# Performance work log

Measured on AMD Instinct MI355X. Metric: run time of the kernel, lower is better.

## Reference

```python
import jax, jax.numpy as jnp
import numpy as np

N, D, NUM_CLASSES = 8192, 64, 16
EPS = 1e-7


def setup_inputs() -> dict:
    key = jax.random.key(0)
    k1, k2 = jax.random.split(key)
    raw = jax.random.normal(k1, (N, D), dtype=jnp.float32)
    # project into the open Poincare ball: norm < 0.9
    nrm = jnp.linalg.norm(raw, axis=-1, keepdims=True)
    points = raw * (0.9 / (1.0 + nrm))
    labels = jax.random.randint(k2, (N,), 0, NUM_CLASSES, dtype=jnp.int64)
    return {"points": points, "labels": labels}


def _poincare_dist_matrix(x):
    # d(x,y) = arccosh(1 + 2||x-y||^2 / ((1-||x||^2)(1-||y||^2)))
    sq = jnp.sum(x * x, axis=-1)                      # [N]
    sqdist = jnp.maximum(sq[:, None] + sq[None, :] - 2.0 * (x @ x.T), 0.0)  # [N,N]
    denom = jnp.maximum((1.0 - sq)[:, None] * (1.0 - sq)[None, :], EPS)
    arg = jnp.maximum(1.0 + 2.0 * sqdist / denom, 1.0 + EPS)
    return jnp.arccosh(arg)


def reference(points, labels):
    d = _poincare_dist_matrix(points)                 # [N,N]
    logits = -d
    n = logits.shape[0]
    diag = jnp.eye(n, dtype=bool)
    neg_inf = jnp.finfo(logits.dtype).min
    # log A_i = logsumexp_{a != i} (-d_ia)
    logA = jax.nn.logsumexp(jnp.where(diag, neg_inf, logits), axis=1)  # [N]
    pos = (labels[:, None] == labels[None, :]) & (~diag)               # [N,N]
    P = jnp.sum(pos, axis=1).astype(logits.dtype)                      # [N]
    p_sum = jnp.sum(jnp.where(pos, logits - logA[:, None], 0.0), axis=1)
    return jnp.sum(-p_sum / P)
```

## Files before the change

### kernel.cpp

```cpp
#include <hip/hip_runtime.h>

#define NPTS 8192
#define DIM 64
#define EPSF 1e-7f
#define LN2F 0.69314718055994531f
#define NBLK 1056

typedef unsigned short u16;
typedef __attribute__((ext_vector_type(8))) short bf16x8;
typedef __attribute__((ext_vector_type(8))) unsigned short u16x8;
typedef __attribute__((ext_vector_type(4))) float f32x4;

__global__ void prep_kernel(const float* __restrict__ x,
                            u16* __restrict__ hi, u16* __restrict__ lo,
                            float* __restrict__ hsq, float* __restrict__ rcpom,
                            float* __restrict__ m4r,
                            float* __restrict__ S, float* __restrict__ T,
                            float* __restrict__ out) {
    int g = blockIdx.x * blockDim.x + threadIdx.x;
    int row = g >> 3, sub = g & 7;
    const float* xp = x + row * DIM + sub * 8;
    float v[8];
    float s = 0.f;
#pragma unroll
    for (int k = 0; k < 8; k++) { v[k] = xp[k]; s = fmaf(v[k], v[k], s); }
    s += __shfl_xor(s, 1);
    s += __shfl_xor(s, 2);
    s += __shfl_xor(s, 4);
    u16x8 h, l;
#pragma unroll
    for (int k = 0; k < 8; k++) {
        unsigned int bits = __float_as_uint(v[k]);
        u16 hb = (u16)(bits >> 16);
        float hf = __uint_as_float(((unsigned int)hb) << 16);
        float lf = v[k] - hf;
        u16 lb = (u16)(__float_as_uint(lf) >> 16);
        h[k] = hb; l[k] = lb;
    }
    *(u16x8*)(hi + row * DIM + sub * 8) = h;
    *(u16x8*)(lo + row * DIM + sub * 8) = l;
    if (sub == 0) {
        float r = 1.0f / (1.0f - s);
        hsq[row] = -0.5f * s;
        rcpom[row] = r;
        m4r[row] = -4.0f * r;
    } else if (sub == 1) {
        S[row] = 0.f;
    } else if (sub == 2) {
        T[row] = 0.f;
    }
    if (g == 3) out[0] = 0.f;
}

__device__ __forceinline__ int cumtiles(int b) { return 65 * b - b * b; }

__global__ void __launch_bounds__(256, 3) pair_mfma(
        const u16* __restrict__ hi, const u16* __restrict__ lo,
        const float* __restrict__ hsq, const float* __restrict__ rcpom,
        const float* __restrict__ m4r, const int* __restrict__ labels,
        float* __restrict__ Sarr, float* __restrict__ Tarr) {
    __shared__ float slabS[4][256], slabT[4][256];

    int tid = threadIdx.x;
    int bid = blockIdx.x;
    int by = (int)((65.0f - __builtin_amdgcn_sqrtf(4225.0f - 4.0f * (float)bid)) * 0.5f);
    while (cumtiles(by + 1) <= bid) by++;
    while (cumtiles(by) > bid) by--;
    int off = bid - cumtiles(by);
    int bx = 2 * by + off;
    bool full = (off >= 2);

    int wave = tid >> 6, lane = tid & 63;
    int quad = lane >> 4, l15 = lane & 15;
    int i0 = bx * 128 + wave * 32;
    int j0 = by * 256;

    bf16x8 a_hi[2][2], a_lo[2][2];
#pragma unroll
    for (int it = 0; it < 2; it++)
#pragma unroll
        for (int ks = 0; ks < 2; ks++) {
            int aoff = (i0 + it * 16 + l15) * DIM + ks * 32 + quad * 8;
            a_hi[it][ks] = *(const bf16x8*)(hi + aoff);
            a_lo[it][ks] = *(const bf16x8*)(lo + aoff);
        }

    float hsqi[8], rcpi[8]; int labi[8];
#pragma unroll
    for (int it = 0; it < 2; it++)
#pragma unroll
        for (int r = 0; r < 4; r++) {
            int row = i0 + it * 16 + quad * 4 + r;
            hsqi[it * 4 + r] = hsq[row];
            rcpi[it * 4 + r] = rcpom[row];
            labi[it * 4 + r] = labels[row];
        }

    if (full) {
        for (int c = tid; c < 256; c += 256) {  }
        slabS[wave][lane] = 0.f;       slabT[wave][lane] = 0.f;
        slabS[wave][lane + 64] = 0.f;  slabT[wave][lane + 64] = 0.f;
        slabS[wave][lane + 128] = 0.f; slabT[wave][lane + 128] = 0.f;
        slabS[wave][lane + 192] = 0.f; slabT[wave][lane + 192] = 0.f;
    }

    float Sx[8], Tx[8];
#pragma unroll
    for (int k = 0; k < 8; k++) { Sx[k] = 0.f; Tx[k] = 0.f; }

#pragma unroll 2
    for (int t = 0; t < 16; t++) {
        int jg = j0 + t * 16 + l15;
        bf16x8 b_hi[2], b_lo[2];
#pragma unroll
        for (int ks = 0; ks < 2; ks++) {
            int boff = jg * DIM + ks * 32 + quad * 8;
            b_hi[ks] = *(const bf16x8*)(hi + boff);
            b_lo[ks] = *(const bf16x8*)(lo + boff);
        }
        float hsqj = hsq[jg];
        float mj = m4r[jg];
        int labj = labels[jg];

        float pS = 0.f, pT = 0.f;
#pragma unroll
        for (int it = 0; it < 2; it++) {
            f32x4 acc0, acc1;
#pragma unroll
            for (int r = 0; r < 4; r++) { acc0[r] = hsqi[it * 4 + r] + hsqj; acc1[r] = 0.f; }
            acc0 = __builtin_amdgcn_mfma_f32_16x16x32_bf16(a_lo[it][0], b_hi[0], acc0, 0, 0, 0);
            acc1 = __builtin_amdgcn_mfma_f32_16x16x32_bf16(a_lo[it][1], b_hi[1], acc1, 0, 0, 0);
            acc0 = __builtin_amdgcn_mfma_f32_16x16x32_bf16(a_hi[it][0], b_lo[0], acc0, 0, 0, 0);
            acc1 = __builtin_amdgcn_mfma_f32_16x16x32_bf16(a_hi[it][1], b_lo[1], acc1, 0, 0, 0);
            acc0 = __builtin_amdgcn_mfma_f32_16x16x32_bf16(a_hi[it][0], b_hi[0], acc0, 0, 0, 0);
            acc1 = __builtin_amdgcn_mfma_f32_16x16x32_bf16(a_hi[it][1], b_hi[1], acc1, 0, 0, 0);

#pragma unroll
            for (int r = 0; r < 4; r++) {
                int idx = it * 4 + r;
                float D = acc0[r] + acc1[r];
                float u = fmaxf(D * rcpi[idx] * mj, EPSF);
                float srt = __builtin_amdgcn_sqrtf(fmaf(u, u, u + u));
                float opu = 1.0f + u;
                float st = opu - srt;
                float l2 = __builtin_amdgcn_logf(opu + srt);
                float tv = (labj == labi[idx]) ? l2 : 0.0f;
                Sx[idx] += st;
                Tx[idx] += tv;
                pS += st; pT += tv;
            }
        }

        if (full) {
            pS += __shfl_xor(pS, 16); pS += __shfl_xor(pS, 32);
            pT += __shfl_xor(pT, 16); pT += __shfl_xor(pT, 32);
            if (quad == 0) {
                int c = t * 16 + l15;
                slabS[wave][c] += pS;
                slabT[wave][c] += pT;
            }
        }
    }

#pragma unroll
    for (int r = 0; r < 8; r++) {
#pragma unroll
        for (int m = 1; m < 16; m <<= 1) {
            Sx[r] += __shfl_xor(Sx[r], m);
            Tx[r] += __shfl_xor(Tx[r], m);
        }
    }
    if (l15 == 0) {
#pragma unroll
        for (int it = 0; it < 2; it++)
#pragma unroll
            for (int r = 0; r < 4; r++) {
                int row = i0 + it * 16 + quad * 4 + r;
                atomicAdd(&Sarr[row], Sx[it * 4 + r]);
                atomicAdd(&Tarr[row], Tx[it * 4 + r]);
            }
    }

    if (full) {
        __syncthreads();
        float s = slabS[0][tid] + slabS[1][tid] + slabS[2][tid] + slabS[3][tid];
        float tt = slabT[0][tid] + slabT[1][tid] + slabT[2][tid] + slabT[3][tid];
        atomicAdd(&Sarr[j0 + tid], s);
        atomicAdd(&Tarr[j0 + tid], tt);
    }
}

__global__ void __launch_bounds__(256) finalize_kernel(
        const float* __restrict__ S, const float* __restrict__ T,
        const int* __restrict__ labels, float* __restrict__ out) {
    __shared__ int hist[16][16];
    __shared__ float cntf[16];
    __shared__ float red[256];
    int tid = threadIdx.x;
    hist[tid >> 4][tid & 15] = 0;
    __syncthreads();
    int rep = tid & 15;
    for (int i = tid; i < NPTS; i += 256)
        atomicAdd(&hist[rep][labels[i]], 1);
    __syncthreads();
    if (tid < 16) {
        int s = 0;
#pragma unroll
        for (int k = 0; k < 16; k++) s += hist[k][tid];
        cntf[tid] = (float)(s - 1);
    }
    __syncthreads();

    float s0 = __builtin_amdgcn_sqrtf(EPSF * (2.0f + EPSF));
    float st0 = 1.0f + EPSF - s0;
    float l20 = __builtin_amdgcn_logf(1.0f + EPSF + s0);
    int i = blockIdx.x * 256 + tid;
    float loss = __logf(S[i] - st0) + (T[i] - l20) * LN2F / cntf[labels[i]];
    red[tid] = loss;
    __syncthreads();
    for (int s = 128; s > 0; s >>= 1) {
        if (tid < s) red[tid] += red[tid + s];
        __syncthreads();
    }
    if (tid == 0) atomicAdd(out, red[0]);
}

extern "C" void kernel_launch(void* const* d_in, const int* in_sizes, int n_in,
                              void* d_out, int out_size, void* d_ws, size_t ws_size,
                              hipStream_t stream) {
    const float* x = (const float*)d_in[0];
    const int* labels = (const int*)d_in[1];

    u16* hi = (u16*)d_ws;
    u16* lo = hi + NPTS * DIM;
    float* hsq = (float*)(lo + NPTS * DIM);
    float* rcpom = hsq + NPTS;
    float* m4r = rcpom + NPTS;
    float* S = m4r + NPTS;
    float* T = S + NPTS;

    prep_kernel<<<(NPTS * 8) / 256, 256, 0, stream>>>(x, hi, lo, hsq, rcpom, m4r, S, T, (float*)d_out);

    pair_mfma<<<NBLK, 256, 0, stream>>>(hi, lo, hsq, rcpom, m4r, labels, S, T);

    finalize_kernel<<<NPTS / 256, 256, 0, stream>>>(S, T, labels, (float*)d_out);
}
```

Baseline: 120.2 us.

## Use persistent blocks with atomic tile counter and pack per-row metadata into float4

The pair kernel becomes persistent: 768 blocks repeatedly take triangular tile indices from a global atomic counter instead of launching one block per tile, which is meant to balance load and cut the tail. Per-point half-square-norm, reciprocal, scaled reciprocal and label are packed into one float4 written by the prep kernel, so each column needs one vector load instead of three scalar loads. The cost is an atomic fetch plus two block barriers per tile, and labels are now compared as floats.

```diff
diff --git a/kernel.cpp b/kernel.cpp
--- a/kernel.cpp
+++ b/kernel.cpp
@@ -5,18 +5,18 @@
 #define EPSF 1e-7f
 #define LN2F 0.69314718055994531f
 #define NBLK 1056
+#define PERSISTENT 768
 
 typedef unsigned short u16;
 typedef __attribute__((ext_vector_type(8))) short bf16x8;
 typedef __attribute__((ext_vector_type(8))) unsigned short u16x8;
 typedef __attribute__((ext_vector_type(4))) float f32x4;
 
-__global__ void prep_kernel(const float* __restrict__ x,
+__global__ void prep_kernel(const float* __restrict__ x, const int* __restrict__ labels,
                             u16* __restrict__ hi, u16* __restrict__ lo,
-                            float* __restrict__ hsq, float* __restrict__ rcpom,
-                            float* __restrict__ m4r,
+                            float4* __restrict__ meta,
                             float* __restrict__ S, float* __restrict__ T,
-                            float* __restrict__ out) {
+                            float* __restrict__ out, int* __restrict__ ctr) {
     int g = blockIdx.x * blockDim.x + threadIdx.x;
     int row = g >> 3, sub = g & 7;
     const float* xp = x + row * DIM + sub * 8;
@@ -41,152 +41,157 @@
     *(u16x8*)(lo + row * DIM + sub * 8) = l;
     if (sub == 0) {
         float r = 1.0f / (1.0f - s);
-        hsq[row] = -0.5f * s;
-        rcpom[row] = r;
-        m4r[row] = -4.0f * r;
+        meta[row] = make_float4(-0.5f * s, r, -4.0f * r, (float)labels[row]);
     } else if (sub == 1) {
         S[row] = 0.f;
     } else if (sub == 2) {
         T[row] = 0.f;
     }
-    if (g == 3) out[0] = 0.f;
+    if (g == 3) { out[0] = 0.f; }
+    if (g == 4) { *ctr = 0; }
 }
 
 __device__ __forceinline__ int cumtiles(int b) { return 65 * b - b * b; }
 
 __global__ void __launch_bounds__(256, 3) pair_mfma(
         const u16* __restrict__ hi, const u16* __restrict__ lo,
-        const float* __restrict__ hsq, const float* __restrict__ rcpom,
-        const float* __restrict__ m4r, const int* __restrict__ labels,
-        float* __restrict__ Sarr, float* __restrict__ Tarr) {
+        const float4* __restrict__ meta,
+        float* __restrict__ Sarr, float* __restrict__ Tarr,
+        int* __restrict__ ctr) {
     __shared__ float slabS[4][256], slabT[4][256];
+    __shared__ int curTile;
 
     int tid = threadIdx.x;
-    int bid = blockIdx.x;
-    int by = (int)((65.0f - __builtin_amdgcn_sqrtf(4225.0f - 4.0f * (float)bid)) * 0.5f);
-    while (cumtiles(by + 1) <= bid) by++;
-    while (cumtiles(by) > bid) by--;
-    int off = bid - cumtiles(by);
-    int bx = 2 * by + off;
-    bool full = (off >= 2);
-
     int wave = tid >> 6, lane = tid & 63;
     int quad = lane >> 4, l15 = lane & 15;
-    int i0 = bx * 128 + wave * 32;
-    int j0 = by * 256;
-
-    bf16x8 a_hi[2][2], a_lo[2][2];
-#pragma unroll
-    for (int it = 0; it < 2; it++)
-#pragma unroll
-        for (int ks = 0; ks < 2; ks++) {
-            int aoff = (i0 + it * 16 + l15) * DIM + ks * 32 + quad * 8;
-            a_hi[it][ks] = *(const bf16x8*)(hi + aoff);
-            a_lo[it][ks] = *(const bf16x8*)(lo + aoff);
-        }
-
-    float hsqi[8], rcpi[8]; int labi[8];
-#pragma unroll
-    for (int it = 0; it < 2; it++)
-#pragma unroll
-        for (int r = 0; r < 4; r++) {
-            int row = i0 + it * 16 + quad * 4 + r;
-            hsqi[it * 4 + r] = hsq[row];
-            rcpi[it * 4 + r] = rcpom[row];
-            labi[it * 4 + r] = labels[row];
-        }
-
-    if (full) {
-        for (int c = tid; c < 256; c += 256) {  }
-        slabS[wave][lane] = 0.f;       slabT[wave][lane] = 0.f;
-        slabS[wave][lane + 64] = 0.f;  slabT[wave][lane + 64] = 0.f;
-        slabS[wave][lane + 128] = 0.f; slabT[wave][lane + 128] = 0.f;
-        slabS[wave][lane + 192] = 0.f; slabT[wave][lane + 192] = 0.f;
-    }
-
-    float Sx[8], Tx[8];
-#pragma unroll
-    for (int k = 0; k < 8; k++) { Sx[k] = 0.f; Tx[k] = 0.f; }
+
+    while (true) {
+        if (tid == 0) curTile = atomicAdd(ctr, 1);
+        __syncthreads();
+        int bid = curTile;
+        if (bid >= NBLK) break;
+
+        int by = (int)((65.0f - __builtin_amdgcn_sqrtf(4225.0f - 4.0f * (float)bid)) * 0.5f);
+        while (cumtiles(by + 1) <= bid) by++;
+        while (cumtiles(by) > bid) by--;
+        int off = bid - cumtiles(by);
+        int bx = 2 * by + off;
+        bool full = (off >= 2);
+
+        int i0 = bx * 128 + wave * 32;
+        int j0 = by * 256;
+
+        bf16x8 a_hi[2][2], a_lo[2][2];
+#pragma unroll
+        for (int it = 0; it < 2; it++)
+#pragma unroll
+            for (int ks = 0; ks < 2; ks++) {
+                int aoff = (i0 + it * 16 + l15) * DIM + ks * 32 + quad * 8;
+                a_hi[it][ks] = *(const bf16x8*)(hi + aoff);
+                a_lo[it][ks] = *(const bf16x8*)(lo + aoff);
+            }
+
+        float hsqi[8], rcpi[8], labi[8];
+#pragma unroll
+        for (int it = 0; it < 2; it++)
+#pragma unroll
+            for (int r = 0; r < 4; r++) {
+                float4 m = meta[i0 + it * 16 + quad * 4 + r];
+                hsqi[it * 4 + r] = m.x;
+                rcpi[it * 4 + r] = m.y;
+                labi[it * 4 + r] = m.w;
+            }
+
+        if (full) {
+            slabS[wave][lane] = 0.f;       slabT[wave][lane] = 0.f;
+            slabS[wave][lane + 64] = 0.f;  slabT[wave][lane + 64] = 0.f;
+            slabS[wave][lane + 128] = 0.f; slabT[wave][lane + 128] = 0.f;
+            slabS[wave][lane + 192] = 0.f; slabT[wave][lane + 192] = 0.f;
+        }
+
+        float Sx[8], Tx[8];
+#pragma unroll
+        for (int k = 0; k < 8; k++) { Sx[k] = 0.f; Tx[k] = 0.f; }
 
 #pragma unroll 2
-    for (int t = 0; t < 16; t++) {
-        int jg = j0 + t * 16 + l15;
-        bf16x8 b_hi[2], b_lo[2];
-#pragma unroll
-        for (int ks = 0; ks < 2; ks++) {
-            int boff = jg * DIM + ks * 32 + quad * 8;
-            b_hi[ks] = *(const bf16x8*)(hi + boff);
-            b_lo[ks] = *(const bf16x8*)(lo + boff);
-        }
-        float hsqj = hsq[jg];
-        float mj = m4r[jg];
-        int labj = labels[jg];
-
-        float pS = 0.f, pT = 0.f;
-#pragma unroll
-        for (int it = 0; it < 2; it++) {
-            f32x4 acc0, acc1;
-#pragma unroll
-            for (int r = 0; r < 4; r++) { acc0[r] = hsqi[it * 4 + r] + hsqj; acc1[r] = 0.f; }
-            acc0 = __builtin_amdgcn_mfma_f32_16x16x32_bf16(a_lo[it][0], b_hi[0], acc0, 0, 0, 0);
-            acc1 = __builtin_amdgcn_mfma_f32_16x16x32_bf16(a_lo[it][1], b_hi[1], acc1, 0, 0, 0);
-            acc0 = __builtin_amdgcn_mfma_f32_16x16x32_bf16(a_hi[it][0], b_lo[0], acc0, 0, 0, 0);
-            acc1 = __builtin_amdgcn_mfma_f32_16x16x32_bf16(a_hi[it][1], b_lo[1], acc1, 0, 0, 0);
-            acc0 = __builtin_amdgcn_mfma_f32_16x16x32_bf16(a_hi[it][0], b_hi[0], acc0, 0, 0, 0);
-            acc1 = __builtin_amdgcn_mfma_f32_16x16x32_bf16(a_hi[it][1], b_hi[1], acc1, 0, 0, 0);
-
-#pragma unroll
-            for (int r = 0; r < 4; r++) {
-                int idx = it * 4 + r;
-                float D = acc0[r] + acc1[r];
-                float u = fmaxf(D * rcpi[idx] * mj, EPSF);
-                float srt = __builtin_amdgcn_sqrtf(fmaf(u, u, u + u));
-                float opu = 1.0f + u;
-                float st = opu - srt;
-                float l2 = __builtin_amdgcn_logf(opu + srt);
-                float tv = (labj == labi[idx]) ? l2 : 0.0f;
-                Sx[idx] += st;
-                Tx[idx] += tv;
-                pS += st; pT += tv;
-            }
+        for (int t = 0; t < 16; t++) {
+            int jg = j0 + t * 16 + l15;
+            bf16x8 b_hi[2], b_lo[2];
+#pragma unroll
+            for (int ks = 0; ks < 2; ks++) {
+                int boff = jg * DIM + ks * 32 + quad * 8;
+                b_hi[ks] = *(const bf16x8*)(hi + boff);
+                b_lo[ks] = *(const bf16x8*)(lo + boff);
+            }
+            float4 mj = meta[jg];
+
+            float pS = 0.f, pT = 0.f;
+#pragma unroll
+            for (int it = 0; it < 2; it++) {
+                f32x4 acc0, acc1;
+#pragma unroll
+                for (int r = 0; r < 4; r++) { acc0[r] = hsqi[it * 4 + r] + mj.x; acc1[r] = 0.f; }
+                acc0 = __builtin_amdgcn_mfma_f32_16x16x32_bf16(a_lo[it][0], b_hi[0], acc0, 0, 0, 0);
+                acc1 = __builtin_amdgcn_mfma_f32_16x16x32_bf16(a_lo[it][1], b_hi[1], acc1, 0, 0, 0);
+                acc0 = __builtin_amdgcn_mfma_f32_16x16x32_bf16(a_hi[it][0], b_lo[0], acc0, 0, 0, 0);
+                acc1 = __builtin_amdgcn_mfma_f32_16x16x32_bf16(a_hi[it][1], b_lo[1], acc1, 0, 0, 0);
+                acc0 = __builtin_amdgcn_mfma_f32_16x16x32_bf16(a_hi[it][0], b_hi[0], acc0, 0, 0, 0);
+                acc1 = __builtin_amdgcn_mfma_f32_16x16x32_bf16(a_hi[it][1], b_hi[1], acc1, 0, 0, 0);
+
+#pragma unroll
+                for (int r = 0; r < 4; r++) {
+                    int idx = it * 4 + r;
+                    float D = acc0[r] + acc1[r];
+                    float u = fmaxf(D * rcpi[idx] * mj.z, EPSF);
+                    float srt = __builtin_amdgcn_sqrtf(fmaf(u, u, u + u));
+                    float opu = 1.0f + u;
+                    float st = opu - srt;
+                    float l2 = __builtin_amdgcn_logf(opu + srt);
+                    float tv = (mj.w == labi[idx]) ? l2 : 0.0f;
+                    Sx[idx] += st;
+                    Tx[idx] += tv;
+                    pS += st; pT += tv;
+                }
+            }
+
+            if (full) {
+                pS += __shfl_xor(pS, 16); pS += __shfl_xor(pS, 32);
+                pT += __shfl_xor(pT, 16); pT += __shfl_xor(pT, 32);
+                if (quad == 0) {
+                    int c = t * 16 + l15;
+                    slabS[wave][c] += pS;
+                    slabT[wave][c] += pT;
+                }
+            }
+        }
+
+#pragma unroll
+        for (int r = 0; r < 8; r++) {
+#pragma unroll
+            for (int m = 1; m < 16; m <<= 1) {
+                Sx[r] += __shfl_xor(Sx[r], m);
+                Tx[r] += __shfl_xor(Tx[r], m);
+            }
+        }
+        if (l15 == 0) {
+#pragma unroll
+            for (int it = 0; it < 2; it++)
+#pragma unroll
+                for (int r = 0; r < 4; r++) {
+                    int row = i0 + it * 16 + quad * 4 + r;
+                    atomicAdd(&Sarr[row], Sx[it * 4 + r]);
+                    atomicAdd(&Tarr[row], Tx[it * 4 + r]);
+                }
         }
 
         if (full) {
-            pS += __shfl_xor(pS, 16); pS += __shfl_xor(pS, 32);
-            pT += __shfl_xor(pT, 16); pT += __shfl_xor(pT, 32);
-            if (quad == 0) {
-                int c = t * 16 + l15;
-                slabS[wave][c] += pS;
-                slabT[wave][c] += pT;
-            }
-        }
-    }
-
-#pragma unroll
-    for (int r = 0; r < 8; r++) {
-#pragma unroll
-        for (int m = 1; m < 16; m <<= 1) {
-            Sx[r] += __shfl_xor(Sx[r], m);
-            Tx[r] += __shfl_xor(Tx[r], m);
-        }
-    }
-    if (l15 == 0) {
-#pragma unroll
-        for (int it = 0; it < 2; it++)
-#pragma unroll
-            for (int r = 0; r < 4; r++) {
-                int row = i0 + it * 16 + quad * 4 + r;
-                atomicAdd(&Sarr[row], Sx[it * 4 + r]);
-                atomicAdd(&Tarr[row], Tx[it * 4 + r]);
-            }
-    }
-
-    if (full) {
+            __syncthreads();
+            float s = slabS[0][tid] + slabS[1][tid] + slabS[2][tid] + slabS[3][tid];
+            float tt = slabT[0][tid] + slabT[1][tid] + slabT[2][tid] + slabT[3][tid];
+            atomicAdd(&Sarr[j0 + tid], s);
+            atomicAdd(&Tarr[j0 + tid], tt);
+        }
         __syncthreads();
-        float s = slabS[0][tid] + slabS[1][tid] + slabS[2][tid] + slabS[3][tid];
-        float tt = slabT[0][tid] + slabT[1][tid] + slabT[2][tid] + slabT[3][tid];
-        atomicAdd(&Sarr[j0 + tid], s);
-        atomicAdd(&Tarr[j0 + tid], tt);
     }
 }
 
@@ -233,15 +238,14 @@
 
     u16* hi = (u16*)d_ws;
     u16* lo = hi + NPTS * DIM;
-    float* hsq = (float*)(lo + NPTS * DIM);
-    float* rcpom = hsq + NPTS;
-    float* m4r = rcpom + NPTS;
-    float* S = m4r + NPTS;
+    float4* meta = (float4*)(lo + NPTS * DIM);
+    float* S = (float*)(meta + NPTS);
     float* T = S + NPTS;
-
-    prep_kernel<<<(NPTS * 8) / 256, 256, 0, stream>>>(x, hi, lo, hsq, rcpom, m4r, S, T, (float*)d_out);
-
-    pair_mfma<<<NBLK, 256, 0, stream>>>(hi, lo, hsq, rcpom, m4r, labels, S, T);
+    int* ctr = (int*)(T + NPTS);
+
+    prep_kernel<<<(NPTS * 8) / 256, 256, 0, stream>>>(x, labels, hi, lo, meta, S, T, (float*)d_out, ctr);
+
+    pair_mfma<<<PERSISTENT, 256, 0, stream>>>(hi, lo, meta, S, T, ctr);
 
     finalize_kernel<<<NPTS / 256, 256, 0, stream>>>(S, T, labels, (float*)d_out);
 }
```

New measurement: 136.4 us. +13.4%, slower.
